# Optimization experiments

Hardware: AMD Instinct MI355X
Metric: run time of the kernel (lower is better)

Reference implementation:

```python
import jax, jax.numpy as jnp
from jax import lax
import numpy as np

REG = 0.1        # entropic regularization
ITERS = 50       # Sinkhorn iterations
DS = 8           # avg-pool downsample factor
EPS = 1e-8


def _avg_pool_scaled(x, d):
    # F.avg_pool2d(x, d) * d**2 == sum over non-overlapping dxd windows
    B, C, H, W = x.shape
    return x.reshape(B, C, H // d, d, W // d, d).mean(axis=(3, 5)) * (d * d)


def _cost_matrix(H, W):
    y = jnp.arange(H, dtype=jnp.float32)
    x = jnp.arange(W, dtype=jnp.float32)
    yy, xx = jnp.meshgrid(y, x, indexing='ij')
    coords = jnp.stack([yy.ravel(), xx.ravel()], axis=1)      # [N, 2]
    diff = coords[:, None, :] - coords[None, :, :]            # [N, N, 2]
    return (diff ** 2).sum(axis=-1)                           # [N, N] squared euclidean


def setup_inputs() -> dict:
    key = jax.random.key(0)
    k1, k2 = jax.random.split(key)
    B, H, W = 16, 512, 512
    pred_density = jax.random.uniform(k1, (B, 1, H, W), dtype=jnp.float32)
    gt_density = jax.random.uniform(k2, (B, 1, H, W), dtype=jnp.float32)
    return {"pred_density": pred_density, "gt_density": gt_density}


def reference(pred_density, gt_density):
    pred = _avg_pool_scaled(pred_density, DS)
    gt = _avg_pool_scaled(gt_density, DS)
    B, _, H, W = pred.shape
    N = H * W

    C = _cost_matrix(H, W)          # [N, N]
    K = jnp.exp(-C / REG)           # Gibbs kernel
    M = K * C                       # so cost = u @ (M @ v) == sum(P * C) without materializing P

    a = pred.reshape(B, N)
    b = gt.reshape(B, N)
    a_sum = jnp.clip(a.sum(axis=1), 1e-8, None)
    b_sum = jnp.clip(b.sum(axis=1), 1e-8, None)
    a_n = a / a_sum[:, None]
    b_n = b / b_sum[:, None]

    def sinkhorn_cost(a1, b1):
        def step(carry, _):
            u, v = carry
            v = b1 / (K.T @ u + EPS)
            u = a1 / (K @ v + EPS)
            return (u, v), None
        (u, v), _ = lax.scan(step, (jnp.ones_like(a1), jnp.zeros_like(b1)),
                             None, length=ITERS)
        # P = u[:,None] * K * v[None,:]; (P*C).sum() = u^T (K*C) v
        return u @ (M @ v)

    costs = jax.vmap(sinkhorn_cost)(a_n, b_n)                 # [B]
    valid = (a_sum > 0.5) & (b_sum > 0.5)
    return jnp.where(valid, costs, 0.0).sum() / B
```

## Files before the change

kernel.cpp:

```cpp
#include <hip/hip_runtime.h>


#define G1 4.5399929762484854e-05f
#define EPSF 1e-8f

__device__ __forceinline__ float dpp_shr1(float x) {
  return __int_as_float(__builtin_amdgcn_update_dpp(0, __float_as_int(x), 0x138, 0xF, 0xF, true));
}
__device__ __forceinline__ float dpp_shl1(float x) {
  return __int_as_float(__builtin_amdgcn_update_dpp(0, __float_as_int(x), 0x130, 0xF, 0xF, true));
}

extern "C" __global__ void __launch_bounds__(256)
ot_pool(const float* __restrict__ pred, const float* __restrict__ gt,
        float* __restrict__ ws_pool, double* __restrict__ ws_part) {
  const int bw    = blockIdx.x >> 4;
  const int which = bw >> 4;
  const int batch = bw & 15;
  const int wi    = ((blockIdx.x & 15) << 8) | threadIdx.x;
  const float* src = (which ? gt : pred) + batch * (512 * 512);

  const int y = wi >> 6, x = wi & 63;
  const float* base = src + (y * 8) * 512 + x * 8;
  float s = 0.f;
#pragma unroll
  for (int dy = 0; dy < 8; ++dy) {
    const float4* r4 = (const float4*)(base + dy * 512);
    float4 p0 = r4[0], p1 = r4[1];
    s += ((p0.x + p0.y) + (p0.z + p0.w)) + ((p1.x + p1.y) + (p1.z + p1.w));
  }
  ws_pool[bw * 4096 + wi] = s;

  double part = (double)s;
#pragma unroll
  for (int off = 32; off > 0; off >>= 1) part += __shfl_down(part, off, 64);
  __shared__ double pr[4];
  if ((threadIdx.x & 63) == 0) pr[threadIdx.x >> 6] = part;
  __syncthreads();
  if (threadIdx.x == 0)
    ws_part[blockIdx.x] = (pr[0] + pr[1]) + (pr[2] + pr[3]);
}

__device__ __forceinline__ void ot_step(const float (&src)[4], float (&dst)[4],
                                        const float (&wt)[4],
                                        float (*rd)[18][64], float (*wr)[18][64],
                                        int wv, int lane) {
  const float up = rd[1][wv][lane];
  const float dn = rd[0][wv + 2][lane];
#pragma unroll
  for (int r = 1; r < 3; ++r) {
    const float s = (dpp_shr1(src[r]) + dpp_shl1(src[r])) + (src[r - 1] + src[r + 1]);
    dst[r] = wt[r] * __builtin_amdgcn_rcpf(__builtin_fmaf(G1, s, src[r]) + EPSF);
  }
  const float s0 = (dpp_shr1(src[0]) + dpp_shl1(src[0])) + (up + src[1]);
  dst[0] = wt[0] * __builtin_amdgcn_rcpf(__builtin_fmaf(G1, s0, src[0]) + EPSF);
  const float s3 = (dpp_shr1(src[3]) + dpp_shl1(src[3])) + (src[2] + dn);
  dst[3] = wt[3] * __builtin_amdgcn_rcpf(__builtin_fmaf(G1, s3, src[3]) + EPSF);
  wr[0][wv + 1][lane] = dst[0];
  wr[1][wv + 1][lane] = dst[3];
  __syncthreads();
}

extern "C" __global__ void __launch_bounds__(1024)
ot_sinkhorn(const float* __restrict__ ws_pool, const double* __restrict__ ws_part,
            float* __restrict__ out) {
  const int batch = blockIdx.x;
  const int lane  = threadIdx.x & 63;
  const int wv    = threadIdx.x >> 6;

  __shared__ float  bnd[2][2][18][64];
  __shared__ double ssh[2];
  __shared__ float  red[16];

  double s = 0.0;
  if (threadIdx.x < 32) {
    const int whichsel = threadIdx.x >> 4;
    const int sub      = threadIdx.x & 15;
    s = ws_part[((whichsel * 16 + batch) << 4) | sub];
  }
  s += __shfl_down(s, 8, 16);
  s += __shfl_down(s, 4, 16);
  s += __shfl_down(s, 2, 16);
  s += __shfl_down(s, 1, 16);
  if (threadIdx.x == 0)  ssh[0] = s;
  if (threadIdx.x == 16) ssh[1] = s;

  if (wv == 0) {
    bnd[0][1][0][lane] = 0.f; bnd[0][0][17][lane] = 0.f;
    bnd[1][1][0][lane] = 0.f; bnd[1][0][17][lane] = 0.f;
  }
  bnd[0][0][wv + 1][lane] = 1.0f;
  bnd[0][1][wv + 1][lane] = 1.0f;
  __syncthreads();

  const float a_sum = (float)ssh[0];
  const float b_sum = (float)ssh[1];
  const float inva = 1.0f / fmaxf(a_sum, 1e-8f);
  const float invb = 1.0f / fmaxf(b_sum, 1e-8f);

  float av[4], bv[4], u[4], v[4];
  const float* pa = ws_pool + batch * 4096;
  const float* pb = ws_pool + 16 * 4096 + batch * 4096;
#pragma unroll
  for (int r = 0; r < 4; ++r) {
    const int idx = (wv * 4 + r) * 64 + lane;
    av[r] = pa[idx] * inva;
    bv[r] = pb[idx] * invb;
    u[r]  = 1.0f;
  }

#pragma unroll 1
  for (int it = 0; it < 50; ++it) {
    ot_step(u, v, bv, bnd[0], bnd[1], wv, lane);
    ot_step(v, u, av, bnd[1], bnd[0], wv, lane);
  }

  const float up = bnd[1][1][wv][lane];
  const float dn = bnd[1][0][wv + 2][lane];
  float acc = 0.f;
#pragma unroll
  for (int r = 0; r < 4; ++r) {
    const float vm = (r == 0) ? up : v[r - 1];
    const float vp = (r == 3) ? dn : v[r + 1];
    const float sN = (dpp_shr1(v[r]) + dpp_shl1(v[r])) + (vm + vp);
    acc = __builtin_fmaf(u[r], sN, acc);
  }
#pragma unroll
  for (int off = 32; off > 0; off >>= 1) acc += __shfl_down(acc, off, 64);
  if (lane == 0) red[wv] = acc;
  __syncthreads();
  if (threadIdx.x == 0) {
    float c = 0.f;
#pragma unroll
    for (int w = 0; w < 16; ++w) c += red[w];
    c *= G1;
    const bool valid = (a_sum > 0.5f) && (b_sum > 0.5f);
    if (valid) atomicAdd(out, c * (1.0f / 16.0f));
  }
}

extern "C" void kernel_launch(void* const* d_in, const int* in_sizes, int n_in,
                              void* d_out, int out_size, void* d_ws, size_t ws_size,
                              hipStream_t stream) {
  (void)in_sizes; (void)n_in; (void)out_size; (void)ws_size;
  const float* pred = (const float*)d_in[0];
  const float* gt   = (const float*)d_in[1];

  float*  ws_pool = (float*)d_ws;
  double* ws_part = (double*)((char*)d_ws + 2 * 16 * 4096 * 4);

  hipLaunchKernelGGL(ot_pool,     dim3(512), dim3(256),  0, stream, pred, gt, ws_pool, ws_part);
  hipLaunchKernelGGL(ot_sinkhorn, dim3(16),  dim3(1024), 0, stream, ws_pool, ws_part, (float*)d_out);
}
```

Before: 110.2 us.

## Shrink Sinkhorn block to four waves with sixteen rows per thread

Each Sinkhorn block now runs 256 threads instead of 1024, and each thread holds 16 grid rows in registers instead of 4. This cuts the number of waves taking part in every per-half-step barrier and reduces shared-memory boundary exchange. Boundary rows are computed and published first so the interior work can overlap the LDS writes before the barrier. The EPS add is folded into an FMA after the reciprocal, with u initialised to 1+EPS to keep the recurrence equivalent. The cost is more serial work per thread and fewer waves to hide latency.

```diff
diff --git a/kernel.cpp b/kernel.cpp
--- a/kernel.cpp
+++ b/kernel.cpp
@@ -41,36 +41,48 @@
     ws_part[blockIdx.x] = (pr[0] + pr[1]) + (pr[2] + pr[3]);
 }
 
-__device__ __forceinline__ void ot_step(const float (&src)[4], float (&dst)[4],
-                                        const float (&wt)[4],
-                                        float (*rd)[18][64], float (*wr)[18][64],
-                                        int wv, int lane) {
+__device__ __forceinline__ void ot_step16(const float (&src)[16], float (&dst)[16],
+                                          const float (&wt)[16],
+                                          float (*rd)[6][64], float (*wr)[6][64],
+                                          int wv, int lane) {
   const float up = rd[1][wv][lane];
   const float dn = rd[0][wv + 2][lane];
 #pragma unroll
-  for (int r = 1; r < 3; ++r) {
+  for (int r = 2; r < 14; ++r) {
     const float s = (dpp_shr1(src[r]) + dpp_shl1(src[r])) + (src[r - 1] + src[r + 1]);
-    dst[r] = wt[r] * __builtin_amdgcn_rcpf(__builtin_fmaf(G1, s, src[r]) + EPSF);
+    dst[r] = __builtin_fmaf(wt[r], __builtin_amdgcn_rcpf(__builtin_fmaf(G1, s, src[r])), EPSF);
   }
-  const float s0 = (dpp_shr1(src[0]) + dpp_shl1(src[0])) + (up + src[1]);
-  dst[0] = wt[0] * __builtin_amdgcn_rcpf(__builtin_fmaf(G1, s0, src[0]) + EPSF);
-  const float s3 = (dpp_shr1(src[3]) + dpp_shl1(src[3])) + (src[2] + dn);
-  dst[3] = wt[3] * __builtin_amdgcn_rcpf(__builtin_fmaf(G1, s3, src[3]) + EPSF);
+  {
+    const float s = (dpp_shr1(src[0]) + dpp_shl1(src[0])) + (up + src[1]);
+    dst[0] = __builtin_fmaf(wt[0], __builtin_amdgcn_rcpf(__builtin_fmaf(G1, s, src[0])), EPSF);
+  }
+  {
+    const float s = (dpp_shr1(src[15]) + dpp_shl1(src[15])) + (src[14] + dn);
+    dst[15] = __builtin_fmaf(wt[15], __builtin_amdgcn_rcpf(__builtin_fmaf(G1, s, src[15])), EPSF);
+  }
   wr[0][wv + 1][lane] = dst[0];
-  wr[1][wv + 1][lane] = dst[3];
+  wr[1][wv + 1][lane] = dst[15];
+  {
+    const float s = (dpp_shr1(src[1]) + dpp_shl1(src[1])) + (src[0] + src[2]);
+    dst[1] = __builtin_fmaf(wt[1], __builtin_amdgcn_rcpf(__builtin_fmaf(G1, s, src[1])), EPSF);
+  }
+  {
+    const float s = (dpp_shr1(src[14]) + dpp_shl1(src[14])) + (src[13] + src[15]);
+    dst[14] = __builtin_fmaf(wt[14], __builtin_amdgcn_rcpf(__builtin_fmaf(G1, s, src[14])), EPSF);
+  }
   __syncthreads();
 }
 
-extern "C" __global__ void __launch_bounds__(1024)
+extern "C" __global__ void __launch_bounds__(256)
 ot_sinkhorn(const float* __restrict__ ws_pool, const double* __restrict__ ws_part,
             float* __restrict__ out) {
   const int batch = blockIdx.x;
   const int lane  = threadIdx.x & 63;
   const int wv    = threadIdx.x >> 6;
 
-  __shared__ float  bnd[2][2][18][64];
+  __shared__ float  bnd[2][2][6][64];
   __shared__ double ssh[2];
-  __shared__ float  red[16];
+  __shared__ float  red[4];
 
   double s = 0.0;
   if (threadIdx.x < 32) {
@@ -86,11 +98,11 @@
   if (threadIdx.x == 16) ssh[1] = s;
 
   if (wv == 0) {
-    bnd[0][1][0][lane] = 0.f; bnd[0][0][17][lane] = 0.f;
-    bnd[1][1][0][lane] = 0.f; bnd[1][0][17][lane] = 0.f;
+    bnd[0][1][0][lane] = 0.f; bnd[0][0][5][lane] = 0.f;
+    bnd[1][1][0][lane] = 0.f; bnd[1][0][5][lane] = 0.f;
   }
-  bnd[0][0][wv + 1][lane] = 1.0f;
-  bnd[0][1][wv + 1][lane] = 1.0f;
+  bnd[0][0][wv + 1][lane] = 1.0f + EPSF;
+  bnd[0][1][wv + 1][lane] = 1.0f + EPSF;
   __syncthreads();
 
   const float a_sum = (float)ssh[0];
@@ -98,30 +110,30 @@
   const float inva = 1.0f / fmaxf(a_sum, 1e-8f);
   const float invb = 1.0f / fmaxf(b_sum, 1e-8f);
 
-  float av[4], bv[4], u[4], v[4];
+  float av[16], bv[16], u[16], v[16];
   const float* pa = ws_pool + batch * 4096;
   const float* pb = ws_pool + 16 * 4096 + batch * 4096;
 #pragma unroll
-  for (int r = 0; r < 4; ++r) {
-    const int idx = (wv * 4 + r) * 64 + lane;
+  for (int r = 0; r < 16; ++r) {
+    const int idx = (wv * 16 + r) * 64 + lane;
     av[r] = pa[idx] * inva;
     bv[r] = pb[idx] * invb;
-    u[r]  = 1.0f;
+    u[r]  = 1.0f + EPSF;
   }
 
 #pragma unroll 1
   for (int it = 0; it < 50; ++it) {
-    ot_step(u, v, bv, bnd[0], bnd[1], wv, lane);
-    ot_step(v, u, av, bnd[1], bnd[0], wv, lane);
+    ot_step16(u, v, bv, bnd[0], bnd[1], wv, lane);
+    ot_step16(v, u, av, bnd[1], bnd[0], wv, lane);
   }
 
   const float up = bnd[1][1][wv][lane];
   const float dn = bnd[1][0][wv + 2][lane];
   float acc = 0.f;
 #pragma unroll
-  for (int r = 0; r < 4; ++r) {
+  for (int r = 0; r < 16; ++r) {
     const float vm = (r == 0) ? up : v[r - 1];
-    const float vp = (r == 3) ? dn : v[r + 1];
+    const float vp = (r == 15) ? dn : v[r + 1];
     const float sN = (dpp_shr1(v[r]) + dpp_shl1(v[r])) + (vm + vp);
     acc = __builtin_fmaf(u[r], sN, acc);
   }
@@ -130,9 +142,7 @@
   if (lane == 0) red[wv] = acc;
   __syncthreads();
   if (threadIdx.x == 0) {
-    float c = 0.f;
-#pragma unroll
-    for (int w = 0; w < 16; ++w) c += red[w];
+    float c = (red[0] + red[1]) + (red[2] + red[3]);
     c *= G1;
     const bool valid = (a_sum > 0.5f) && (b_sum > 0.5f);
     if (valid) atomicAdd(out, c * (1.0f / 16.0f));
@@ -150,5 +160,5 @@
   double* ws_part = (double*)((char*)d_ws + 2 * 16 * 4096 * 4);
 
   hipLaunchKernelGGL(ot_pool,     dim3(512), dim3(256),  0, stream, pred, gt, ws_pool, ws_part);
-  hipLaunchKernelGGL(ot_sinkhorn, dim3(16),  dim3(1024), 0, stream, ws_pool, ws_part, (float*)d_out);
+  hipLaunchKernelGGL(ot_sinkhorn, dim3(16),  dim3(256),  0, stream, ws_pool, ws_part, (float*)d_out);
 }
```

Result: faster. 106.7 us (-3.2%).
